# Performance work log

Measured on AMD Instinct MI355X. Metric: run time of the kernel, lower is better.

The kernel has to match this reference:

```python
import jax, jax.numpy as jnp
import numpy as np


def setup_inputs() -> dict:
    key = jax.random.key(0)
    k1, k2 = jax.random.split(key)
    B, S, H, E = 4, 4096, 4096, 64
    hidden_states = jax.random.normal(k1, (B, S, H), dtype=jnp.float32)
    weight = jax.random.normal(k2, (E, H), dtype=jnp.float32) * 0.02
    return {"hidden_states": hidden_states, "weight": weight, "top_k": 8}


def reference(hidden_states, weight, top_k):
    # router logits: (B, S, E) = hidden @ weight.T, computed in fp32 as in torch path
    router_logits = jnp.einsum(
        "bsh,eh->bse",
        hidden_states.astype(jnp.float32),
        weight.astype(jnp.float32),
    )
    topk_weights, topk_indices = jax.lax.top_k(router_logits, top_k)
    topk_weights = jax.nn.softmax(topk_weights, axis=-1)
    return router_logits, topk_indices, topk_weights
```

## Files before the change

kernel.cpp:

```cpp
#include <hip/hip_runtime.h>
#include <math.h>

#define TOKENS 16384
#define HDIM   4096
#define NEXP   64
#define TOPK   8

#define BM 32
#define BK 32
#define LDA 33
#define CHUNKS (HDIM / BK)

typedef double f64x4 __attribute__((ext_vector_type(4)));

__global__ __launch_bounds__(256) void router_gemm_mfma(const float* __restrict__ hid,
                                                        const float* __restrict__ wgt,
                                                        float* __restrict__ logits) {
    __shared__ double As[2][BM * LDA];
    __shared__ double Ws[2][NEXP * LDA];

    const int tid  = threadIdx.x;
    const int bm   = blockIdx.x * BM;

    const int wv   = tid >> 6;
    const int lane = tid & 63;
    const int tg   = wv & 1;
    const int eh   = wv >> 1;
    const int r    = lane & 15;
    const int kq   = lane >> 4;

    f64x4 rowp = {0., 0., 0., 0.};
    f64x4 colp = {0., 0., 0., 0.};
    rowp = __builtin_amdgcn_mfma_f64_16x16x4f64((double)r, 1.0, rowp, 0, 0, 0);
    colp = __builtin_amdgcn_mfma_f64_16x16x4f64(1.0, (double)r, colp, 0, 0, 0);
    int drow[4], dcol[4];
#pragma unroll
    for (int j = 0; j < 4; ++j) {
        drow[j] = (int)(rowp[j] * 0.25 + 0.5);
        dcol[j] = (int)(colp[j] * 0.25 + 0.5);
    }

    f64x4 acc0 = {0., 0., 0., 0.};
    f64x4 acc1 = {0., 0., 0., 0.};

    const int arow = tid >> 3;
    const int aq   = tid & 7;
    const int wrow = tid >> 3;
    const int wq   = tid & 7;

    float4 pa, pw0, pw1;

    pa  = *reinterpret_cast<const float4*>(&hid[(size_t)(bm + arow) * HDIM + aq * 4]);
    pw0 = *reinterpret_cast<const float4*>(&wgt[(size_t)wrow * HDIM + wq * 4]);
    pw1 = *reinterpret_cast<const float4*>(&wgt[(size_t)(wrow + 32) * HDIM + wq * 4]);
    {
        double* a = &As[0][arow * LDA + aq * 4];
        a[0] = pa.x; a[1] = pa.y; a[2] = pa.z; a[3] = pa.w;
        double* w0 = &Ws[0][wrow * LDA + wq * 4];
        w0[0] = pw0.x; w0[1] = pw0.y; w0[2] = pw0.z; w0[3] = pw0.w;
        double* w1 = &Ws[0][(wrow + 32) * LDA + wq * 4];
        w1[0] = pw1.x; w1[1] = pw1.y; w1[2] = pw1.z; w1[3] = pw1.w;
    }

    int cur = 0;
    for (int c = 0; c < CHUNKS; ++c) {
        __syncthreads();

        if (c + 1 < CHUNKS) {
            const int k0n = (c + 1) * BK;
            pa  = *reinterpret_cast<const float4*>(&hid[(size_t)(bm + arow) * HDIM + k0n + aq * 4]);
            pw0 = *reinterpret_cast<const float4*>(&wgt[(size_t)wrow * HDIM + k0n + wq * 4]);
            pw1 = *reinterpret_cast<const float4*>(&wgt[(size_t)(wrow + 32) * HDIM + k0n + wq * 4]);
        }

        const double* Ab  = &As[cur][(tg * 16 + r) * LDA + kq];
        const double* Wb0 = &Ws[cur][(eh * 32 + r) * LDA + kq];
        const double* Wb1 = Wb0 + 16 * LDA;
#pragma unroll
        for (int ks = 0; ks < 8; ++ks) {
            double a  = Ab[ks * 4];
            double b0 = Wb0[ks * 4];
            double b1 = Wb1[ks * 4];
            acc0 = __builtin_amdgcn_mfma_f64_16x16x4f64(a, b0, acc0, 0, 0, 0);
            acc1 = __builtin_amdgcn_mfma_f64_16x16x4f64(a, b1, acc1, 0, 0, 0);
        }

        if (c + 1 < CHUNKS) {
            double* a = &As[cur ^ 1][arow * LDA + aq * 4];
            a[0] = pa.x; a[1] = pa.y; a[2] = pa.z; a[3] = pa.w;
            double* w0 = &Ws[cur ^ 1][wrow * LDA + wq * 4];
            w0[0] = pw0.x; w0[1] = pw0.y; w0[2] = pw0.z; w0[3] = pw0.w;
            double* w1 = &Ws[cur ^ 1][(wrow + 32) * LDA + wq * 4];
            w1[0] = pw1.x; w1[1] = pw1.y; w1[2] = pw1.z; w1[3] = pw1.w;
        }
        cur ^= 1;
    }

#pragma unroll
    for (int j = 0; j < 4; ++j) {
        const int row = bm + tg * 16 + drow[j];
        const int c0  = eh * 32 + dcol[j];
        logits[(size_t)row * NEXP + c0]      = (float)acc0[j];
        logits[(size_t)row * NEXP + c0 + 16] = (float)acc1[j];
    }
}

__global__ __launch_bounds__(256) void topk_softmax(const float* __restrict__ logits,
                                                    float* __restrict__ out_idx,
                                                    float* __restrict__ out_w) {
    const int wave  = threadIdx.x >> 6;
    const int lane  = threadIdx.x & 63;
    const int token = blockIdx.x * 4 + wave;
    if (token >= TOKENS) return;

    float v = logits[(size_t)token * NEXP + lane];

    float myval = 0.f;
    int   myidx = 0;
    float max0  = 0.f;

#pragma unroll
    for (int k = 0; k < TOPK; ++k) {
        float bv = v;
        int   bi = lane;
#pragma unroll
        for (int off = 32; off > 0; off >>= 1) {
            float ov = __shfl_xor(bv, off);
            int   oi = __shfl_xor(bi, off);
            if (ov > bv || (ov == bv && oi < bi)) { bv = ov; bi = oi; }
        }
        if (k == 0) max0 = bv;
        if (lane == k) { myval = bv; myidx = bi; }
        if (lane == bi) v = -INFINITY;
    }

    float e = (lane < TOPK) ? expf(myval - max0) : 0.f;
    float s = e;
#pragma unroll
    for (int off = 4; off > 0; off >>= 1) s += __shfl_xor(s, off);

    if (lane < TOPK) {
        size_t o = (size_t)token * TOPK + lane;
        out_idx[o] = (float)myidx;
        out_w[o]   = e / s;
    }
}

extern "C" void kernel_launch(void* const* d_in, const int* in_sizes, int n_in,
                              void* d_out, int out_size, void* d_ws, size_t ws_size,
                              hipStream_t stream) {
    const float* hid = (const float*)d_in[0];
    const float* wgt = (const float*)d_in[1];

    float* logits  = (float*)d_out;
    float* out_idx = logits + (size_t)TOKENS * NEXP;
    float* out_w   = out_idx + (size_t)TOKENS * TOPK;

    router_gemm_mfma<<<TOKENS / BM, 256, 0, stream>>>(hid, wgt, logits);
    topk_softmax<<<TOKENS / 4, 256, 0, stream>>>(logits, out_idx, out_w);
}
```

Measured before the change: 193.1 us.

## Halve row tile and keep fp32 staging in LDS with vector stores

```diff
diff --git a/kernel.cpp b/kernel.cpp
--- a/kernel.cpp
+++ b/kernel.cpp
@@ -6,9 +6,9 @@
 #define NEXP   64
 #define TOPK   8
 
-#define BM 32
+#define BM 16
 #define BK 32
-#define LDA 33
+#define LDF 36
 #define CHUNKS (HDIM / BK)
 
 typedef double f64x4 __attribute__((ext_vector_type(4)));
@@ -16,16 +16,13 @@
 __global__ __launch_bounds__(256) void router_gemm_mfma(const float* __restrict__ hid,
                                                         const float* __restrict__ wgt,
                                                         float* __restrict__ logits) {
-    __shared__ double As[2][BM * LDA];
-    __shared__ double Ws[2][NEXP * LDA];
+    __shared__ float As[2][BM * LDF];
+    __shared__ float Bs[2][NEXP * LDF];
 
     const int tid  = threadIdx.x;
     const int bm   = blockIdx.x * BM;
-
     const int wv   = tid >> 6;
     const int lane = tid & 63;
-    const int tg   = wv & 1;
-    const int eh   = wv >> 1;
     const int r    = lane & 15;
     const int kq   = lane >> 4;
 
@@ -40,27 +37,21 @@
         dcol[j] = (int)(colp[j] * 0.25 + 0.5);
     }
 
-    f64x4 acc0 = {0., 0., 0., 0.};
-    f64x4 acc1 = {0., 0., 0., 0.};
+    f64x4 acc = {0., 0., 0., 0.};
 
     const int arow = tid >> 3;
-    const int aq   = tid & 7;
-    const int wrow = tid >> 3;
-    const int wq   = tid & 7;
+    const int af   = tid & 7;
+    const int brow = tid >> 3;
+    const int bf   = tid & 7;
 
-    float4 pa, pw0, pw1;
+    float4 pa, pb0, pb1;
 
-    pa  = *reinterpret_cast<const float4*>(&hid[(size_t)(bm + arow) * HDIM + aq * 4]);
-    pw0 = *reinterpret_cast<const float4*>(&wgt[(size_t)wrow * HDIM + wq * 4]);
-    pw1 = *reinterpret_cast<const float4*>(&wgt[(size_t)(wrow + 32) * HDIM + wq * 4]);
-    {
-        double* a = &As[0][arow * LDA + aq * 4];
-        a[0] = pa.x; a[1] = pa.y; a[2] = pa.z; a[3] = pa.w;
-        double* w0 = &Ws[0][wrow * LDA + wq * 4];
-        w0[0] = pw0.x; w0[1] = pw0.y; w0[2] = pw0.z; w0[3] = pw0.w;
-        double* w1 = &Ws[0][(wrow + 32) * LDA + wq * 4];
-        w1[0] = pw1.x; w1[1] = pw1.y; w1[2] = pw1.z; w1[3] = pw1.w;
-    }
+    if (tid < 128) pa = *reinterpret_cast<const float4*>(&hid[(size_t)(bm + arow) * HDIM + af * 4]);
+    pb0 = *reinterpret_cast<const float4*>(&wgt[(size_t)brow * HDIM + bf * 4]);
+    pb1 = *reinterpret_cast<const float4*>(&wgt[(size_t)(brow + 32) * HDIM + bf * 4]);
+    if (tid < 128) *reinterpret_cast<float4*>(&As[0][arow * LDF + af * 4]) = pa;
+    *reinterpret_cast<float4*>(&Bs[0][brow * LDF + bf * 4])        = pb0;
+    *reinterpret_cast<float4*>(&Bs[0][(brow + 32) * LDF + bf * 4]) = pb1;
 
     int cur = 0;
     for (int c = 0; c < CHUNKS; ++c) {
@@ -68,40 +59,33 @@
 
         if (c + 1 < CHUNKS) {
             const int k0n = (c + 1) * BK;
-            pa  = *reinterpret_cast<const float4*>(&hid[(size_t)(bm + arow) * HDIM + k0n + aq * 4]);
-            pw0 = *reinterpret_cast<const float4*>(&wgt[(size_t)wrow * HDIM + k0n + wq * 4]);
-            pw1 = *reinterpret_cast<const float4*>(&wgt[(size_t)(wrow + 32) * HDIM + k0n + wq * 4]);
+            if (tid < 128) pa = *reinterpret_cast<const float4*>(&hid[(size_t)(bm + arow) * HDIM + k0n + af * 4]);
+            pb0 = *reinterpret_cast<const float4*>(&wgt[(size_t)brow * HDIM + k0n + bf * 4]);
+            pb1 = *reinterpret_cast<const float4*>(&wgt[(size_t)(brow + 32) * HDIM + k0n + bf * 4]);
         }
 
-        const double* Ab  = &As[cur][(tg * 16 + r) * LDA + kq];
-        const double* Wb0 = &Ws[cur][(eh * 32 + r) * LDA + kq];
-        const double* Wb1 = Wb0 + 16 * LDA;
+        const float* Ab = &As[cur][r * LDF + kq];
+        const float* Bb = &Bs[cur][(wv * 16 + r) * LDF + kq];
 #pragma unroll
         for (int ks = 0; ks < 8; ++ks) {
-            double a  = Ab[ks * 4];
-            double b0 = Wb0[ks * 4];
-            double b1 = Wb1[ks * 4];
-            acc0 = __builtin_amdgcn_mfma_f64_16x16x4f64(a, b0, acc0, 0, 0, 0);
-            acc1 = __builtin_amdgcn_mfma_f64_16x16x4f64(a, b1, acc1, 0, 0, 0);
+            double a = (double)Ab[ks * 4];
+            double b = (double)Bb[ks * 4];
+            acc = __builtin_amdgcn_mfma_f64_16x16x4f64(a, b, acc, 0, 0, 0);
         }
 
         if (c + 1 < CHUNKS) {
-            double* a = &As[cur ^ 1][arow * LDA + aq * 4];
-            a[0] = pa.x; a[1] = pa.y; a[2] = pa.z; a[3] = pa.w;
-            double* w0 = &Ws[cur ^ 1][wrow * LDA + wq * 4];
-            w0[0] = pw0.x; w0[1] = pw0.y; w0[2] = pw0.z; w0[3] = pw0.w;
-            double* w1 = &Ws[cur ^ 1][(wrow + 32) * LDA + wq * 4];
-            w1[0] = pw1.x; w1[1] = pw1.y; w1[2] = pw1.z; w1[3] = pw1.w;
+            if (tid < 128) *reinterpret_cast<float4*>(&As[cur ^ 1][arow * LDF + af * 4]) = pa;
+            *reinterpret_cast<float4*>(&Bs[cur ^ 1][brow * LDF + bf * 4])        = pb0;
+            *reinterpret_cast<float4*>(&Bs[cur ^ 1][(brow + 32) * LDF + bf * 4]) = pb1;
         }
         cur ^= 1;
     }
 
 #pragma unroll
     for (int j = 0; j < 4; ++j) {
-        const int row = bm + tg * 16 + drow[j];
-        const int c0  = eh * 32 + dcol[j];
-        logits[(size_t)row * NEXP + c0]      = (float)acc0[j];
-        logits[(size_t)row * NEXP + c0 + 16] = (float)acc1[j];
+        const int row = bm + drow[j];
+        const int col = wv * 16 + dcol[j];
+        logits[(size_t)row * NEXP + col] = (float)acc[j];
     }
 }
 
```

Measured after the change: 196.1 us. Within noise of the previous version (+1.5%).
